# Kernel tuning notes

Measured on AMD Instinct MI355X. Metric: run time of the kernel, lower is better.

Reference implementation:

```python
import jax, jax.numpy as jnp
import numpy as np

NUM_HEADS = 12
EMBED_DIM = 768


def setup_inputs() -> dict:
    key = jax.random.key(0)
    ks = jax.random.split(key, 7)
    B, N, E = 4, 2048, EMBED_DIM
    s = 1.0 / np.sqrt(E)  # init scale to keep activations sane
    return {
        "x": jax.random.normal(ks[0], (B, N, E), dtype=jnp.float32),
        "Wq": jax.random.normal(ks[1], (E, E), dtype=jnp.float32) * s,
        "bq": jnp.zeros((E,), dtype=jnp.float32),
        "Wk": jax.random.normal(ks[2], (E, E), dtype=jnp.float32) * s,
        "bk": jnp.zeros((E,), dtype=jnp.float32),
        "Wv": jax.random.normal(ks[3], (E, E), dtype=jnp.float32) * s,
        "bv": jnp.zeros((E,), dtype=jnp.float32),
    }


def reference(x, Wq, bq, Wk, bk, Wv, bv):
    B, N, E = x.shape
    H = NUM_HEADS
    d = E // H
    # QKV projections, split into heads: b n (h d) -> b h n d
    q = (x @ Wq + bq).reshape(B, N, H, d).transpose(0, 2, 1, 3)
    k = (x @ Wk + bk).reshape(B, N, H, d).transpose(0, 2, 1, 3)
    v = (x @ Wv + bv).reshape(B, N, H, d).transpose(0, 2, 1, 3)
    # NOTE: non-standard scale = 1/sqrt(num_heads), not 1/sqrt(head_dim)
    scale = 1.0 / jnp.sqrt(jnp.asarray(H, dtype=x.dtype))
    attn_weight = jnp.einsum("bhqd,bhkd->bhqk", q, k) * scale
    # NOTE: softmax over the QUERY axis (dim=2), not the key axis
    attn_score = jax.nn.softmax(attn_weight, axis=2)
    out = jnp.einsum("bhqk,bhkd->bhqd", attn_score, v)
    # b h n d -> b n (h d)
    return out.transpose(0, 2, 1, 3).reshape(B, N, E)
```

## Files before the change

kernel.cpp:

```cpp
#include <hip/hip_runtime.h>

#define NN 2048
#define EE 768
#define HH 12
#define DD 64
#define BHX 48
#define MM 8192

typedef unsigned short u16;
typedef unsigned int u32;
typedef __attribute__((ext_vector_type(8))) short bf16x8;
typedef __attribute__((ext_vector_type(4))) float f32x4;

#if __has_builtin(__builtin_amdgcn_exp2f)
#define EX2(x) __builtin_amdgcn_exp2f(x)
#else
#define EX2(x) exp2f(x)
#endif

#define MFMA16(a, b, c) __builtin_amdgcn_mfma_f32_16x16x32_bf16((a), (b), (c), 0, 0, 0)

__device__ __forceinline__ u16 f2bf(float f) {
    u32 u = __builtin_bit_cast(u32, f);
    u32 r = (u + 0x7FFFu + ((u >> 16) & 1u)) >> 16;
    return (u16)r;
}
__device__ __forceinline__ float bf2f(u16 b) {
    u32 u = ((u32)b) << 16;
    return __builtin_bit_cast(float, u);
}
__device__ __forceinline__ u32 pack_rn(float a, float b) {
    u32 ua = __builtin_bit_cast(u32, a) + 0x8000u;
    u32 ub = __builtin_bit_cast(u32, b) + 0x8000u;
    return (ub & 0xFFFF0000u) | (ua >> 16);
}
__device__ __forceinline__ void gload_lds16(const u16* g, u16* l) {
    __builtin_amdgcn_global_load_lds((const __attribute__((address_space(1))) void*)g,
                                     (__attribute__((address_space(3))) void*)l, 16, 0, 0);
}

__global__ __launch_bounds__(256) void k_cvt_x(const float* __restrict__ x, u16* __restrict__ xb, int n8) {
    int i = blockIdx.x * 256 + threadIdx.x;
    if (i >= n8) return;
    const float4* x4 = (const float4*)x;
    float4 a = x4[i * 2], b = x4[i * 2 + 1];
    uint4 o;
    o.x = (u32)f2bf(a.x) | ((u32)f2bf(a.y) << 16);
    o.y = (u32)f2bf(a.z) | ((u32)f2bf(a.w) << 16);
    o.z = (u32)f2bf(b.x) | ((u32)f2bf(b.y) << 16);
    o.w = (u32)f2bf(b.z) | ((u32)f2bf(b.w) << 16);
    ((uint4*)xb)[i] = o;
}

__global__ __launch_bounds__(256) void k_wt(const float* __restrict__ Wq, const float* __restrict__ Wk,
                                            const float* __restrict__ Wv, u16* __restrict__ wt) {
    __shared__ u16 lt[64 * 80];
    const int z = blockIdx.z;
    const float* W = (z == 0) ? Wq : (z == 1 ? Wk : Wv);
    const int k0 = blockIdx.x * 64, j0 = blockIdx.y * 64;
    const int tid = threadIdx.x;
#pragma unroll
    for (int p = 0; p < 4; ++p) {
        int c = p * 256 + tid;
        int kk = c >> 4, j4 = (c & 15) * 4;
        float4 v = *(const float4*)(W + (size_t)(k0 + kk) * EE + j0 + j4);
        lt[(j4 + 0) * 80 + kk] = f2bf(v.x);
        lt[(j4 + 1) * 80 + kk] = f2bf(v.y);
        lt[(j4 + 2) * 80 + kk] = f2bf(v.z);
        lt[(j4 + 3) * 80 + kk] = f2bf(v.w);
    }
    __syncthreads();
    u16* dstz = wt + (size_t)z * EE * EE;
#pragma unroll
    for (int p = 0; p < 2; ++p) {
        int c = p * 256 + tid;
        int j = c >> 3, kc = c & 7;
        uint4 o = *(const uint4*)&lt[j * 80 + kc * 8];
        *(uint4*)(dstz + (size_t)(j0 + j) * EE + k0 + kc * 8) = o;
    }
}

__global__ __launch_bounds__(256) void k_proj(const u16* __restrict__ xb, const u16* __restrict__ wt,
                                              const float* __restrict__ bq, const float* __restrict__ bk,
                                              const float* __restrict__ bv, u16* __restrict__ qh,
                                              u16* __restrict__ kh, u16* __restrict__ vh) {
    __shared__ u16 lA[128 * 32];
    __shared__ u16 lB[128 * 32];
    const int z = blockIdx.z;
    const u16* Wz = wt + (size_t)z * EE * EE;
    const float* bias = (z == 0) ? bq : (z == 1 ? bk : bv);
    u16* outp = (z == 0) ? qh : (z == 1 ? kh : vh);
    const float oscale = (z == 0) ? (0.28867513459481287f * 1.4426950408889634f) : 1.0f;
    const int tid = threadIdx.x;
    const int lane = tid & 63, w = tid >> 6;
    const int wr = w >> 1, wc = w & 1, lr = lane & 15, lg = lane >> 4;
    const int m0 = blockIdx.x * 128, n0 = blockIdx.y * 128;

    f32x4 acc[4][4];
#pragma unroll
    for (int mi = 0; mi < 4; mi++)
#pragma unroll
        for (int ni = 0; ni < 4; ni++) acc[mi][ni] = (f32x4){0.f, 0.f, 0.f, 0.f};

    for (int kt = 0; kt < EE; kt += 32) {
#pragma unroll
        for (int i = 0; i < 2; i++) {
            int c = i * 256 + tid;
            int row = c >> 2, cc = c & 3;
            gload_lds16(xb + (size_t)(m0 + row) * EE + kt + cc * 8, &lA[c * 8]);
            gload_lds16(Wz + (size_t)(n0 + row) * EE + kt + cc * 8, &lB[c * 8]);
        }
        __syncthreads();
        bf16x8 af[4], bfr[4];
#pragma unroll
        for (int mi = 0; mi < 4; mi++) af[mi] = *(const bf16x8*)&lA[(wr * 64 + mi * 16 + lr) * 32 + lg * 8];
#pragma unroll
        for (int ni = 0; ni < 4; ni++) bfr[ni] = *(const bf16x8*)&lB[(wc * 64 + ni * 16 + lr) * 32 + lg * 8];
#pragma unroll
        for (int mi = 0; mi < 4; mi++)
#pragma unroll
            for (int ni = 0; ni < 4; ni++) acc[mi][ni] = MFMA16(af[mi], bfr[ni], acc[mi][ni]);
        __syncthreads();
    }

#pragma unroll
    for (int ni = 0; ni < 4; ni++) {
        int col = n0 + wc * 64 + ni * 16 + lr;
        float bb = bias[col];
        int h = col >> 6, dd = col & 63;
#pragma unroll
        for (int mi = 0; mi < 4; mi++) {
            int rowbase = m0 + wr * 64 + mi * 16 + lg * 4;
#pragma unroll
            for (int r = 0; r < 4; r++) {
                int row = rowbase + r;
                int b = row >> 11, nn = row & 2047;
                outp[(((size_t)b * HH + h) * NN + nn) * DD + dd] = f2bf((acc[mi][ni][r] + bb) * oscale);
            }
        }
    }
}

__global__ __launch_bounds__(512) void k_stats(const u16* __restrict__ qh, const u16* __restrict__ kh,
                                               float* __restrict__ rlb) {
    __shared__ u16 lds[2][4096];
    const int lin = blockIdx.x;
    const int nb = (lin & 7) * 96 + (lin >> 3);
    const int bh = nb >> 4, kb = nb & 15;
    const int tid = threadIdx.x, lane = tid & 63, w = tid >> 6;
    const int lr = lane & 15, lg = lane >> 4;
    const int kw0 = kb * 128 + w * 16;
    const u16* Q = qh + (size_t)bh * NN * DD;
    const u16* K = kh + (size_t)bh * NN * DD;

    bf16x8 kf[2];
#pragma unroll
    for (int kk = 0; kk < 2; kk++)
        kf[kk] = *(const bf16x8*)(K + (size_t)(kw0 + lr) * DD + kk * 32 + lg * 8);

    const int c = tid;
    const int f = c >> 6;
    const int qrow = (f >> 1) * 16 + (c & 15);
    const int doff = (f & 1) * 32 + ((c >> 4) & 3) * 8;
    const u16* qp = Q + (size_t)qrow * DD + doff;

#define STAGE_Q(buf, q0) gload_lds16(qp + (size_t)(q0) * DD, &lds[buf][c * 8])

    STAGE_Q(0, 0);
    __syncthreads();
    float lacc = 0.f;
    int cur = 0;
    for (int it = 0; it < 32; ++it) {
        if (it < 31) STAGE_Q(cur ^ 1, (it + 1) * 64);
#pragma unroll
        for (int qt = 0; qt < 4; ++qt) {
            bf16x8 qa0 = *(const bf16x8*)&lds[cur][(qt * 2 + 0) * 512 + lane * 8];
            bf16x8 qa1 = *(const bf16x8*)&lds[cur][(qt * 2 + 1) * 512 + lane * 8];
            f32x4 ss = (f32x4){0.f, 0.f, 0.f, 0.f};
            ss = MFMA16(qa0, kf[0], ss);
            ss = MFMA16(qa1, kf[1], ss);
            lacc += EX2(ss[0]) + EX2(ss[1]) + EX2(ss[2]) + EX2(ss[3]);
        }
        __syncthreads();
        cur ^= 1;
    }
#undef STAGE_Q
    float v = lacc;
    v += __shfl_xor(v, 16);
    v += __shfl_xor(v, 32);
    if (lane < 16) rlb[(size_t)bh * NN + kw0 + lane] = 1.0f / v;
}

__global__ __launch_bounds__(256) void k_vtrans(const u16* __restrict__ vh, const float* __restrict__ rlb,
                                                u16* __restrict__ vt) {
    __shared__ u16 lds[64 * 80];
    const int bh = blockIdx.x, n0 = blockIdx.y * 64;
    const int tid = threadIdx.x;
    const u16* src = vh + (size_t)bh * NN * DD + (size_t)n0 * DD;
    const float* rlp = rlb + (size_t)bh * NN + n0;
#pragma unroll
    for (int i = 0; i < 2; i++) {
        int c = i * 256 + tid;
        int row = c >> 3, dc = c & 7;
        uint4 vraw = *(const uint4*)(src + row * DD + dc * 8);
        float rk = rlp[row];
        u32 uu[4] = {vraw.x, vraw.y, vraw.z, vraw.w};
#pragma unroll
        for (int j = 0; j < 4; j++) {
            u16 e0 = (u16)(uu[j] & 0xffff), e1 = (u16)(uu[j] >> 16);
            lds[(dc * 8 + 2 * j) * 80 + row] = f2bf(rk * bf2f(e0));
            lds[(dc * 8 + 2 * j + 1) * 80 + row] = f2bf(rk * bf2f(e1));
        }
    }
    __syncthreads();
    u16* dst = vt + (size_t)bh * DD * NN + n0;
#pragma unroll
    for (int i = 0; i < 2; i++) {
        int c = i * 256 + tid;
        int d = c >> 3, nc = c & 7;
        int w0 = nc * 8;
        uint2 a = *(const uint2*)&lds[d * 80 + w0];
        uint2 b = *(const uint2*)&lds[d * 80 + w0 + 4];
        int hi32 = (w0 >> 5) * 32;
        int wa = w0 & 31, wb = (w0 + 4) & 31;
        int ca = ((wa & 15) >> 2) * 8 + (wa >> 4) * 4;
        int cb = ((wb & 15) >> 2) * 8 + (wb >> 4) * 4;
        *(uint2*)(dst + (size_t)d * NN + hi32 + ca) = a;
        *(uint2*)(dst + (size_t)d * NN + hi32 + cb) = b;
    }
}

__global__ __launch_bounds__(512) void k_attn(const u16* __restrict__ qh, const u16* __restrict__ kh,
                                              const u16* __restrict__ vt, float* __restrict__ out) {
    __shared__ u16 lds[2][8192];
    const int lin = blockIdx.x;
    const int nb = (lin & 7) * 96 + (lin >> 3);
    const int bh = nb >> 4, qb = nb & 15;
    const int tid = threadIdx.x, lane = tid & 63, w = tid >> 6;
    const int lr = lane & 15, lg = lane >> 4;
    const int qw0 = qb * 128 + w * 16;
    const u16* Q = qh + (size_t)bh * NN * DD;
    const u16* K = kh + (size_t)bh * NN * DD;
    const u16* V = vt + (size_t)bh * DD * NN;

    bf16x8 qf[2];
#pragma unroll
    for (int kk = 0; kk < 2; kk++)
        qf[kk] = *(const bf16x8*)(Q + (size_t)(qw0 + lr) * DD + kk * 32 + lg * 8);

    const int c = tid;
    const int f = c >> 6;
    const int rk = (f >> 2) * 32 + ((f >> 1) & 1) * 16 + (c & 15);
    const int doff = (f & 1) * 32 + ((c >> 4) & 3) * 8;
    const u16* kp = K + (size_t)rk * DD + doff;
    const int drow = (f & 3) * 16 + (c & 15);
    const int koff = (f >> 2) * 32 + ((c >> 4) & 3) * 8;
    const u16* vp = V + (size_t)drow * NN + koff;

#define STAGE_KV(buf, k0)                                          \
    do {                                                           \
        gload_lds16(kp + (size_t)(k0) * DD, &lds[buf][c * 8]);     \
        gload_lds16(vp + (size_t)(k0), &lds[buf][4096 + c * 8]);   \
    } while (0)

    f32x4 acc[4];
#pragma unroll
    for (int di = 0; di < 4; di++) acc[di] = (f32x4){0.f, 0.f, 0.f, 0.f};

    STAGE_KV(0, 0);
    __syncthreads();
    int cur = 0;
    for (int it = 0; it < 32; ++it) {
        if (it < 31) STAGE_KV(cur ^ 1, (it + 1) * 64);
        const u16* Lk = &lds[cur][0];
        const u16* Lv = &lds[cur][4096];
#pragma unroll
        for (int kc = 0; kc < 2; ++kc) {
            bf16x8 kf2[2][2];
#pragma unroll
            for (int t = 0; t < 2; t++)
#pragma unroll
                for (int kk = 0; kk < 2; kk++)
                    kf2[t][kk] = *(const bf16x8*)&Lk[((kc * 2 + t) * 2 + kk) * 512 + lane * 8];
            bf16x8 vf[4];
#pragma unroll
            for (int di = 0; di < 4; di++)
                vf[di] = *(const bf16x8*)&Lv[(kc * 4 + di) * 512 + lane * 8];
            f32x4 s0 = (f32x4){0.f, 0.f, 0.f, 0.f}, s1 = (f32x4){0.f, 0.f, 0.f, 0.f};
            s0 = MFMA16(kf2[0][0], qf[0], s0);
            s0 = MFMA16(kf2[0][1], qf[1], s0);
            s1 = MFMA16(kf2[1][0], qf[0], s1);
            s1 = MFMA16(kf2[1][1], qf[1], s1);
            uint4 pu;
            pu.x = pack_rn(EX2(s0[0]), EX2(s0[1]));
            pu.y = pack_rn(EX2(s0[2]), EX2(s0[3]));
            pu.z = pack_rn(EX2(s1[0]), EX2(s1[1]));
            pu.w = pack_rn(EX2(s1[2]), EX2(s1[3]));
            bf16x8 pa = __builtin_bit_cast(bf16x8, pu);
#pragma unroll
            for (int di = 0; di < 4; di++) acc[di] = MFMA16(pa, vf[di], acc[di]);
        }
        __syncthreads();
        cur ^= 1;
    }
#undef STAGE_KV

    const int b = bh / HH, h = bh % HH;
#pragma unroll
    for (int di = 0; di < 4; di++)
#pragma unroll
        for (int r = 0; r < 4; r++) {
            int q = qw0 + lg * 4 + r;
            int d = di * 16 + lr;
            out[((size_t)(b * NN + q)) * EE + h * DD + d] = acc[di][r];
        }
}

extern "C" void kernel_launch(void* const* d_in, const int* in_sizes, int n_in,
                              void* d_out, int out_size, void* d_ws, size_t ws_size,
                              hipStream_t stream) {
    const float* x = (const float*)d_in[0];
    const float* Wq = (const float*)d_in[1];
    const float* bq = (const float*)d_in[2];
    const float* Wk = (const float*)d_in[3];
    const float* bk = (const float*)d_in[4];
    const float* Wv = (const float*)d_in[5];
    const float* bv = (const float*)d_in[6];
    float* out = (float*)d_out;
    char* ws = (char*)d_ws;

    size_t off = 0;
    u16* xb = (u16*)(ws + off); off += (size_t)MM * EE * 2;
    u16* wt = (u16*)(ws + off); off += (size_t)3 * EE * EE * 2;
    u16* qh = (u16*)(ws + off); off += (size_t)BHX * NN * DD * 2;
    u16* kh = (u16*)(ws + off); off += (size_t)BHX * NN * DD * 2;
    u16* vh = (u16*)(ws + off); off += (size_t)BHX * NN * DD * 2;
    u16* vt = (u16*)(ws + off); off += (size_t)BHX * NN * DD * 2;
    float* rlb = (float*)(ws + off); off += (size_t)BHX * NN * 4;

    k_cvt_x<<<dim3(3072), dim3(256), 0, stream>>>(x, xb, MM * EE / 8);
    k_wt<<<dim3(12, 12, 3), dim3(256), 0, stream>>>(Wq, Wk, Wv, wt);
    k_proj<<<dim3(64, 6, 3), dim3(256), 0, stream>>>(xb, wt, bq, bk, bv, qh, kh, vh);
    k_stats<<<dim3(768), dim3(512), 0, stream>>>(qh, kh, rlb);
    k_vtrans<<<dim3(48, 32), dim3(256), 0, stream>>>(vh, rlb, vt);
    k_attn<<<dim3(768), dim3(512), 0, stream>>>(qh, kh, vt, out);
}
```

Measured before the change: 169.7 us.

## Split k_stats query range in halves and process two key tiles per wave

New measurement: 191.1 us. 12.6% more time.

```diff
diff --git a/kernel.cpp b/kernel.cpp
--- a/kernel.cpp
+++ b/kernel.cpp
@@ -142,21 +142,23 @@
 }
 
 __global__ __launch_bounds__(512) void k_stats(const u16* __restrict__ qh, const u16* __restrict__ kh,
-                                               float* __restrict__ rlb) {
+                                               float* __restrict__ lsum) {
     __shared__ u16 lds[2][4096];
     const int lin = blockIdx.x;
     const int nb = (lin & 7) * 96 + (lin >> 3);
-    const int bh = nb >> 4, kb = nb & 15;
+    const int qs = nb & 1, kb = (nb >> 1) & 7, bh = nb >> 4;
     const int tid = threadIdx.x, lane = tid & 63, w = tid >> 6;
     const int lr = lane & 15, lg = lane >> 4;
-    const int kw0 = kb * 128 + w * 16;
-    const u16* Q = qh + (size_t)bh * NN * DD;
+    const int kw0 = kb * 256 + w * 32;
+    const u16* Q = qh + (size_t)bh * NN * DD + (size_t)(qs * 1024) * DD;
     const u16* K = kh + (size_t)bh * NN * DD;
 
-    bf16x8 kf[2];
-#pragma unroll
-    for (int kk = 0; kk < 2; kk++)
-        kf[kk] = *(const bf16x8*)(K + (size_t)(kw0 + lr) * DD + kk * 32 + lg * 8);
+    bf16x8 kf[2][2];
+#pragma unroll
+    for (int t = 0; t < 2; t++)
+#pragma unroll
+        for (int kk = 0; kk < 2; kk++)
+            kf[t][kk] = *(const bf16x8*)(K + (size_t)(kw0 + t * 16 + lr) * DD + kk * 32 + lg * 8);
 
     const int c = tid;
     const int f = c >> 6;
@@ -168,42 +170,50 @@
 
     STAGE_Q(0, 0);
     __syncthreads();
-    float lacc = 0.f;
+    float lacc[2] = {0.f, 0.f};
     int cur = 0;
-    for (int it = 0; it < 32; ++it) {
-        if (it < 31) STAGE_Q(cur ^ 1, (it + 1) * 64);
+    for (int it = 0; it < 16; ++it) {
+        if (it < 15) STAGE_Q(cur ^ 1, (it + 1) * 64);
 #pragma unroll
         for (int qt = 0; qt < 4; ++qt) {
             bf16x8 qa0 = *(const bf16x8*)&lds[cur][(qt * 2 + 0) * 512 + lane * 8];
             bf16x8 qa1 = *(const bf16x8*)&lds[cur][(qt * 2 + 1) * 512 + lane * 8];
-            f32x4 ss = (f32x4){0.f, 0.f, 0.f, 0.f};
-            ss = MFMA16(qa0, kf[0], ss);
-            ss = MFMA16(qa1, kf[1], ss);
-            lacc += EX2(ss[0]) + EX2(ss[1]) + EX2(ss[2]) + EX2(ss[3]);
+#pragma unroll
+            for (int t = 0; t < 2; t++) {
+                f32x4 ss = (f32x4){0.f, 0.f, 0.f, 0.f};
+                ss = MFMA16(qa0, kf[t][0], ss);
+                ss = MFMA16(qa1, kf[t][1], ss);
+                lacc[t] += EX2(ss[0]) + EX2(ss[1]) + EX2(ss[2]) + EX2(ss[3]);
+            }
         }
         __syncthreads();
         cur ^= 1;
     }
 #undef STAGE_Q
-    float v = lacc;
-    v += __shfl_xor(v, 16);
-    v += __shfl_xor(v, 32);
-    if (lane < 16) rlb[(size_t)bh * NN + kw0 + lane] = 1.0f / v;
-}
-
-__global__ __launch_bounds__(256) void k_vtrans(const u16* __restrict__ vh, const float* __restrict__ rlb,
+#pragma unroll
+    for (int t = 0; t < 2; t++) {
+        float v = lacc[t];
+        v += __shfl_xor(v, 16);
+        v += __shfl_xor(v, 32);
+        if (lane < 16)
+            lsum[(size_t)qs * BHX * NN + (size_t)bh * NN + kw0 + t * 16 + lane] = v;
+    }
+}
+
+__global__ __launch_bounds__(256) void k_vtrans(const u16* __restrict__ vh, const float* __restrict__ lsum,
                                                 u16* __restrict__ vt) {
     __shared__ u16 lds[64 * 80];
     const int bh = blockIdx.x, n0 = blockIdx.y * 64;
     const int tid = threadIdx.x;
     const u16* src = vh + (size_t)bh * NN * DD + (size_t)n0 * DD;
-    const float* rlp = rlb + (size_t)bh * NN + n0;
+    const float* l0 = lsum + (size_t)bh * NN + n0;
+    const float* l1 = lsum + (size_t)BHX * NN + (size_t)bh * NN + n0;
 #pragma unroll
     for (int i = 0; i < 2; i++) {
         int c = i * 256 + tid;
         int row = c >> 3, dc = c & 7;
         uint4 vraw = *(const uint4*)(src + row * DD + dc * 8);
-        float rk = rlp[row];
+        float rk = 1.0f / (l0[row] + l1[row]);
         u32 uu[4] = {vraw.x, vraw.y, vraw.z, vraw.w};
 #pragma unroll
         for (int j = 0; j < 4; j++) {
@@ -336,12 +346,12 @@
     u16* kh = (u16*)(ws + off); off += (size_t)BHX * NN * DD * 2;
     u16* vh = (u16*)(ws + off); off += (size_t)BHX * NN * DD * 2;
     u16* vt = (u16*)(ws + off); off += (size_t)BHX * NN * DD * 2;
-    float* rlb = (float*)(ws + off); off += (size_t)BHX * NN * 4;
+    float* lsum = (float*)(ws + off); off += (size_t)2 * BHX * NN * 4;
 
     k_cvt_x<<<dim3(3072), dim3(256), 0, stream>>>(x, xb, MM * EE / 8);
     k_wt<<<dim3(12, 12, 3), dim3(256), 0, stream>>>(Wq, Wk, Wv, wt);
     k_proj<<<dim3(64, 6, 3), dim3(256), 0, stream>>>(xb, wt, bq, bk, bv, qh, kh, vh);
-    k_stats<<<dim3(768), dim3(512), 0, stream>>>(qh, kh, rlb);
-    k_vtrans<<<dim3(48, 32), dim3(256), 0, stream>>>(vh, rlb, vt);
+    k_stats<<<dim3(768), dim3(512), 0, stream>>>(qh, kh, lsum);
+    k_vtrans<<<dim3(48, 32), dim3(256), 0, stream>>>(vh, lsum, vt);
     k_attn<<<dim3(768), dim3(512), 0, stream>>>(qh, kh, vt, out);
 }
```
